# Kernel optimization log

Measured on AMD Instinct MI355X. Metric: run time of the kernel, lower is better.

Reference implementation:

```python
import jax, jax.numpy as jnp
import numpy as np

B, N, E, K = 8, 4096, 1, 3
F = [16, 32, 16]
MLP_HID, MLP_OUT = 64, 1


def graph_filter(x, S, h, b):
    # x: [B, Fin, N], S: [E, N, N], h: [Fout, E, K, Fin], b: [Fout, 1]
    Bx, Fin, Nx = x.shape
    Ex, Kx = h.shape[1], h.shape[2]
    cur = jnp.broadcast_to(x[:, None], (Bx, Ex, Fin, Nx))  # tap 0: z = x
    zs = [cur]
    for _ in range(Kx - 1):
        cur = jnp.einsum('enm,befm->befn', S, cur)  # diffuse one hop
        zs.append(cur)
    z = jnp.stack(zs, axis=2)  # [B, E, K, Fin, N]
    return jnp.einsum('gekf,bekfn->bgn', h, z) + b[None]  # [B, Fout, N]


def gnn_layer(x, S, h, b, n_out):
    # GraphFilter -> ReLU -> NoPool (select first n_out nodes)
    return jax.nn.relu(graph_filter(x, S, h, b))[:, :, :n_out]


def setup_inputs() -> dict:
    key = jax.random.key(0)
    ks = jax.random.split(key, 16)
    sN = np.float32(1.0 / np.sqrt(N))
    x = jax.random.normal(ks[0], (B, F[0], N), dtype=jnp.float32)
    S_clique = jax.random.normal(ks[1], (E, N, N), dtype=jnp.float32) * sN
    S_line = jax.random.normal(ks[2], (E, N, N), dtype=jnp.float32) * sN

    def w(k, fo, fi):
        s = np.float32(1.0 / np.sqrt(fi * K))
        return jax.random.normal(k, (fo, E, K, fi), dtype=jnp.float32) * s

    Wc1, bc1 = w(ks[3], F[1], F[0]), jnp.zeros((F[1], 1), jnp.float32)
    Wc2, bc2 = w(ks[4], F[2], F[1]), jnp.zeros((F[2], 1), jnp.float32)
    Wl1, bl1 = w(ks[5], F[1], F[0]), jnp.zeros((F[1], 1), jnp.float32)
    Wl2, bl2 = w(ks[6], F[2], F[1]), jnp.zeros((F[2], 1), jnp.float32)
    d_in = N * F[-1]
    Wm1 = jax.random.normal(ks[7], (MLP_HID, d_in), dtype=jnp.float32) * np.float32(1.0 / np.sqrt(d_in))
    bm1 = jnp.zeros((MLP_HID,), jnp.float32)
    Wm2 = jax.random.normal(ks[8], (MLP_OUT, MLP_HID), dtype=jnp.float32) * np.float32(1.0 / np.sqrt(MLP_HID))
    bm2 = jnp.zeros((MLP_OUT,), jnp.float32)
    return {'x': x, 'S_clique': S_clique, 'S_line': S_line,
            'Wc1': Wc1, 'bc1': bc1, 'Wc2': Wc2, 'bc2': bc2,
            'Wl1': Wl1, 'bl1': bl1, 'Wl2': Wl2, 'bl2': bl2,
            'Wm1': Wm1, 'bm1': bm1, 'Wm2': Wm2, 'bm2': bm2}


def reference(x, S_clique, S_line, Wc1, bc1, Wc2, bc2, Wl1, bl1, Wl2, bl2, Wm1, bm1, Wm2, bm2):
    # clique-expansion branch (L=2 layers)
    y = gnn_layer(x, S_clique, Wc1, bc1, N)
    y = gnn_layer(y, S_clique, Wc2, bc2, N)
    # line-expansion branch (L=2 layers)
    y = gnn_layer(y, S_line, Wl1, bl1, N)
    y = gnn_layer(y, S_line, Wl2, bl2, N)
    yFlat = y.reshape(y.shape[0], -1)  # [B, F[-1]*N] (row-major matches torch)
    h = jax.nn.relu(yFlat @ Wm1.T + bm1)
    return h @ Wm2.T + bm2  # [B, 1]
```

## Files before the change

### kernel.cpp

```cpp
#include <hip/hip_runtime.h>


#define NN 4096
#define BB 8

typedef unsigned short u16;
typedef unsigned int   u32;

typedef __attribute__((ext_vector_type(8))) short bf16x8;
typedef __attribute__((ext_vector_type(4))) float f32x4;

__device__ __forceinline__ u16 f2bf(float f) {
    union { float f; u32 i; } c; c.f = f;
    u32 i = c.i;
    u32 r = (i + 0x7FFFu + ((i >> 16) & 1u)) >> 16;
    return (u16)r;
}
__device__ __forceinline__ float bf2f(u16 u) {
    union { u32 i; float f; } c; c.i = ((u32)u) << 16; return c.f;
}

__device__ __forceinline__ void gload_lds16(const u16* g, u16* l) {
    __builtin_amdgcn_global_load_lds(
        (__attribute__((address_space(1))) void*)g,
        (__attribute__((address_space(3))) void*)l, 16, 0, 0);
}

__global__ __launch_bounds__(256) void cvt3(const float* __restrict__ a, u16* __restrict__ da, int na,
                                            const float* __restrict__ b, u16* __restrict__ db, int nb,
                                            const float* __restrict__ c, u16* __restrict__ dc, int nc)
{
    const int tot = (na + nb + nc) >> 2;
    for (int q = blockIdx.x * 256 + threadIdx.x; q < tot; q += gridDim.x * 256) {
        const int i = q << 2;
        const float* s; u16* d;
        if (i < na)           { s = a + i;            d = da + i; }
        else if (i < na + nb) { s = b + (i - na);     d = db + (i - na); }
        else                  { s = c + (i - na - nb); d = dc + (i - na - nb); }
        float4 v = *(const float4*)s;
        ushort4 o;
        o.x = f2bf(v.x); o.y = f2bf(v.y); o.z = f2bf(v.z); o.w = f2bf(v.w);
        *(ushort4*)d = o;
    }
}

template <int ITERS>
__global__ __launch_bounds__(256) void diffuse(const u16* __restrict__ Z,
                                               const u16* __restrict__ S,
                                               u16* __restrict__ Part)
{
    __shared__ u16 As[3 * 128 * 64];
    __shared__ u16 Bs[3 * 64 * 64];

    const int bx    = blockIdx.x;
    const int ntile = ((bx & 7) << 3) | (bx >> 3);
    const int nBase = ntile * 64;
    const int mBase = blockIdx.y * 128;
    const int tid   = threadIdx.x;
    const int lane  = tid & 63;
    const int wv    = tid >> 6;
    const int quad  = lane >> 4;
    const int l16   = lane & 15;

    const int kStart = (int)blockIdx.z * (ITERS * 64);

    const int rl   = lane >> 3;
    const int gsl  = lane & 7;
    const int gsrc = gsl ^ rl;

    f32x4 acc[2][4];
#pragma unroll
    for (int i = 0; i < 2; ++i)
#pragma unroll
        for (int j = 0; j < 4; ++j) acc[i][j] = (f32x4){0.f, 0.f, 0.f, 0.f};

    auto stage = [&](int buf, int k0) {
#pragma unroll
        for (int j = 0; j < 4; ++j) {
            const int rb = (wv * 4 + j) * 8;
            gload_lds16(Z + (size_t)(mBase + rb + rl) * NN + k0 + gsrc * 8,
                        &As[buf * 8192 + rb * 64]);
        }
#pragma unroll
        for (int j = 0; j < 2; ++j) {
            const int rb = (wv * 2 + j) * 8;
            gload_lds16(S + (size_t)(nBase + rb + rl) * NN + k0 + gsrc * 8,
                        &Bs[buf * 4096 + rb * 64]);
        }
    };

    auto compute = [&](int buf) {
#pragma unroll
        for (int s = 0; s < 2; ++s) {
            const int g = s * 4 + quad;
            bf16x8 af[2], bf[4];
#pragma unroll
            for (int mi = 0; mi < 2; ++mi) {
                const int r = wv * 32 + mi * 16 + l16;
                af[mi] = *(const bf16x8*)&As[buf * 8192 + r * 64 + ((g ^ (r & 7)) << 3)];
            }
#pragma unroll
            for (int ni = 0; ni < 4; ++ni) {
                const int r = ni * 16 + l16;
                bf[ni] = *(const bf16x8*)&Bs[buf * 4096 + r * 64 + ((g ^ (r & 7)) << 3)];
            }
#pragma unroll
            for (int mi = 0; mi < 2; ++mi)
#pragma unroll
                for (int ni = 0; ni < 4; ++ni)
                    acc[mi][ni] = __builtin_amdgcn_mfma_f32_16x16x32_bf16(
                        af[mi], bf[ni], acc[mi][ni], 0, 0, 0);
        }
    };

    stage(0, kStart);
    stage(1, kStart + 64);

#pragma unroll
    for (int i = 0; i < ITERS; ++i) {
        if (i + 2 < ITERS) stage((i + 2) % 3, kStart + (i + 2) * 64);
        if (i < ITERS - 2)
            asm volatile("s_waitcnt vmcnt(12)" ::: "memory");
        else if (i == ITERS - 2)
            asm volatile("s_waitcnt vmcnt(6)" ::: "memory");
        else
            asm volatile("s_waitcnt vmcnt(0)" ::: "memory");
        __builtin_amdgcn_s_barrier();
        compute(i % 3);
        if (i + 1 < ITERS) __builtin_amdgcn_s_barrier();
    }

    asm volatile("s_waitcnt lgkmcnt(0)" ::: "memory");
    __builtin_amdgcn_s_barrier();

    u16* tb = &As[wv * 2304];
#pragma unroll
    for (int mi = 0; mi < 2; ++mi)
#pragma unroll
        for (int ni = 0; ni < 4; ++ni)
#pragma unroll
            for (int i = 0; i < 4; ++i)
                tb[(mi * 16 + quad * 4 + i) * 72 + ni * 16 + l16] =
                    f2bf(acc[mi][ni][i]);

    const size_t plane = (size_t)gridDim.y * 128 * NN;
    u16* pp = Part + (size_t)blockIdx.z * plane;
    const int row0g = mBase + wv * 32;
#pragma unroll
    for (int j = 0; j < 4; ++j) {
        const int r = (lane >> 3) + j * 8;
        const int c = (lane & 7) * 8;
        bf16x8 v = *(const bf16x8*)&tb[r * 72 + c];
        *(bf16x8*)&pp[(size_t)(row0g + r) * NN + nBase + c] = v;
    }
}

template <int KS>
__global__ __launch_bounds__(256) void reduce_part(const u16* __restrict__ part,
                                                   int planeElems,
                                                   u16* __restrict__ outb)
{
    const int base   = (blockIdx.x * 256 + threadIdx.x) * 8;
    const int stride = gridDim.x * 256 * 8;
    for (int i = base; i < planeElems; i += stride) {
        float s[8];
#pragma unroll
        for (int e = 0; e < 8; ++e) s[e] = 0.f;
#pragma unroll
        for (int p = 0; p < KS; ++p) {
            uint4 v = *(const uint4*)(part + (size_t)p * planeElems + i);
            const u32 w[4] = {v.x, v.y, v.z, v.w};
#pragma unroll
            for (int q = 0; q < 4; ++q) {
                union { u32 i; float f; } lo, hi;
                lo.i = w[q] << 16;
                hi.i = w[q] & 0xFFFF0000u;
                s[q * 2]     += lo.f;
                s[q * 2 + 1] += hi.f;
            }
        }
        uint4 o;
        o.x = (u32)f2bf(s[0]) | ((u32)f2bf(s[1]) << 16);
        o.y = (u32)f2bf(s[2]) | ((u32)f2bf(s[3]) << 16);
        o.z = (u32)f2bf(s[4]) | ((u32)f2bf(s[5]) << 16);
        o.w = (u32)f2bf(s[6]) | ((u32)f2bf(s[7]) << 16);
        *(uint4*)(outb + i) = o;
    }
}

template <int FIN, int FOUT, int KS>
__global__ __launch_bounds__(256) void combine_relu(
    const u16* __restrict__ z0, const u16* __restrict__ z1,
    const u16* __restrict__ part2, int planeElems,
    const float* __restrict__ W, const float* __restrict__ bias,
    u16* __restrict__ out)
{
    __shared__ float hs[FOUT * 3 * FIN];
    __shared__ float bs[FOUT];
    for (int i = threadIdx.x; i < FOUT * 3 * FIN; i += 256) hs[i] = W[i];
    if (threadIdx.x < FOUT) bs[threadIdx.x] = bias[threadIdx.x];
    __syncthreads();

    const int nb = NN / 256;
    const int b  = blockIdx.x / nb;
    const int n  = (blockIdx.x % nb) * 256 + threadIdx.x;

    float zv[3][FIN];
    const u16* zp0 = z0 + (size_t)b * FIN * NN + n;
    const u16* zp1 = z1 + (size_t)b * FIN * NN + n;
    const u16* zp2 = part2 + (size_t)b * FIN * NN + n;
#pragma unroll
    for (int f = 0; f < FIN; ++f) {
        zv[0][f] = bf2f(zp0[(size_t)f * NN]);
        zv[1][f] = bf2f(zp1[(size_t)f * NN]);
        float s = 0.f;
#pragma unroll
        for (int p = 0; p < KS; ++p)
            s += bf2f(zp2[(size_t)p * planeElems + (size_t)f * NN]);
        zv[2][f] = s;
    }

    u16* op = out + (size_t)b * FOUT * NN + n;
    for (int g = 0; g < FOUT; ++g) {
        float acc = bs[g];
#pragma unroll
        for (int k = 0; k < 3; ++k)
#pragma unroll
            for (int f = 0; f < FIN; ++f)
                acc = fmaf(hs[(g * 3 + k) * FIN + f], zv[k][f], acc);
        op[(size_t)g * NN] = f2bf(fmaxf(acc, 0.f));
    }
}

__global__ __launch_bounds__(256) void mlp1(const u16* __restrict__ y,
                                            const float* __restrict__ Wm1,
                                            float* __restrict__ h1p)
{
    const int j    = blockIdx.x;
    const int base = blockIdx.y * 8192;
    const int D    = 16 * NN;

    float acc[BB];
#pragma unroll
    for (int b = 0; b < BB; ++b) acc[b] = 0.f;

    const float* wrow = Wm1 + (size_t)j * D + base;
    for (int idx = threadIdx.x * 8; idx < 8192; idx += 256 * 8) {
        float4 w0 = *(const float4*)(wrow + idx);
        float4 w1 = *(const float4*)(wrow + idx + 4);
#pragma unroll
        for (int b = 0; b < BB; ++b) {
            uint4 yv = *(const uint4*)(y + (size_t)b * D + base + idx);
            union { u32 i; float f; } c[8];
            c[0].i = yv.x << 16; c[1].i = yv.x & 0xFFFF0000u;
            c[2].i = yv.y << 16; c[3].i = yv.y & 0xFFFF0000u;
            c[4].i = yv.z << 16; c[5].i = yv.z & 0xFFFF0000u;
            c[6].i = yv.w << 16; c[7].i = yv.w & 0xFFFF0000u;
            acc[b] = fmaf(w0.x, c[0].f, acc[b]);
            acc[b] = fmaf(w0.y, c[1].f, acc[b]);
            acc[b] = fmaf(w0.z, c[2].f, acc[b]);
            acc[b] = fmaf(w0.w, c[3].f, acc[b]);
            acc[b] = fmaf(w1.x, c[4].f, acc[b]);
            acc[b] = fmaf(w1.y, c[5].f, acc[b]);
            acc[b] = fmaf(w1.z, c[6].f, acc[b]);
            acc[b] = fmaf(w1.w, c[7].f, acc[b]);
        }
    }

    __shared__ float red[BB][4];
    const int lane = threadIdx.x & 63;
    const int w    = threadIdx.x >> 6;
#pragma unroll
    for (int b = 0; b < BB; ++b) {
        float v = acc[b];
        for (int off = 32; off > 0; off >>= 1) v += __shfl_down(v, off, 64);
        if (lane == 0) red[b][w] = v;
    }
    __syncthreads();
    if (threadIdx.x < BB) {
        const int b = threadIdx.x;
        h1p[blockIdx.y * (BB * 64) + b * 64 + j] =
            red[b][0] + red[b][1] + red[b][2] + red[b][3];
    }
}

__global__ void mlp2(const float* __restrict__ h1p,
                     const float* __restrict__ bm1,
                     const float* __restrict__ Wm2,
                     const float* __restrict__ bm2, float* __restrict__ out)
{
    const int lane = threadIdx.x;
    const float w    = Wm2[lane];
    const float b1   = bm1[lane];
    const float bias = bm2[0];
    for (int b = 0; b < BB; ++b) {
        float h = 0.f;
#pragma unroll
        for (int p = 0; p < 8; ++p) h += h1p[p * (BB * 64) + b * 64 + lane];
        float v = fmaxf(h + b1, 0.f) * w;
        for (int off = 32; off > 0; off >>= 1) v += __shfl_down(v, off, 64);
        if (lane == 0) out[b] = v + bias;
    }
}

extern "C" void kernel_launch(void* const* d_in, const int* in_sizes, int n_in,
                              void* d_out, int out_size, void* d_ws, size_t ws_size,
                              hipStream_t stream)
{
    const float* x   = (const float*)d_in[0];
    const float* Sc  = (const float*)d_in[1];
    const float* Sl  = (const float*)d_in[2];
    const float* Wc1 = (const float*)d_in[3];
    const float* bc1 = (const float*)d_in[4];
    const float* Wc2 = (const float*)d_in[5];
    const float* bc2 = (const float*)d_in[6];
    const float* Wl1 = (const float*)d_in[7];
    const float* bl1 = (const float*)d_in[8];
    const float* Wl2 = (const float*)d_in[9];
    const float* bl2 = (const float*)d_in[10];
    const float* Wm1 = (const float*)d_in[11];
    const float* bm1 = (const float*)d_in[12];
    const float* Wm2 = (const float*)d_in[13];
    const float* bm2 = (const float*)d_in[14];
    float* out = (float*)d_out;

    char* ws = (char*)d_ws;
    u16*   part = (u16*)(ws);
    u16*   zb1  = (u16*)(ws + (8u  << 20));
    u16*   yPa  = (u16*)(ws + (12u << 20));
    u16*   yPb  = (u16*)(ws + (14u << 20));
    float* h1p  = (float*)(ws + (16u << 20));
    u16*   Scb  = (u16*)(ws + (17u << 20));
    u16*   Slb  = Scb + (size_t)NN * NN;

    const dim3 blk(256);
    const dim3 gridCmb(BB * NN / 256);
    const dim3 g2(64, 1, 8);
    const dim3 g4(64, 2, 4);
    const int  pl128 = 128 * NN;
    const int  pl256 = 256 * NN;

    cvt3<<<2048, blk, 0, stream>>>(Sc, Scb, NN * NN, Sl, Slb, NN * NN,
                                   x, yPa, 128 * NN);

    diffuse<8><<<g2, blk, 0, stream>>>(yPa, Scb, part);
    reduce_part<8><<<256, blk, 0, stream>>>(part, pl128, zb1);
    diffuse<8><<<g2, blk, 0, stream>>>(zb1, Scb, part);
    combine_relu<16, 32, 8><<<gridCmb, blk, 0, stream>>>(yPa, zb1, part, pl128,
                                                         Wc1, bc1, yPb);
    diffuse<16><<<g4, blk, 0, stream>>>(yPb, Scb, part);
    reduce_part<4><<<512, blk, 0, stream>>>(part, pl256, zb1);
    diffuse<16><<<g4, blk, 0, stream>>>(zb1, Scb, part);
    combine_relu<32, 16, 4><<<gridCmb, blk, 0, stream>>>(yPb, zb1, part, pl256,
                                                         Wc2, bc2, yPa);
    diffuse<8><<<g2, blk, 0, stream>>>(yPa, Slb, part);
    reduce_part<8><<<256, blk, 0, stream>>>(part, pl128, zb1);
    diffuse<8><<<g2, blk, 0, stream>>>(zb1, Slb, part);
    combine_relu<16, 32, 8><<<gridCmb, blk, 0, stream>>>(yPa, zb1, part, pl128,
                                                         Wl1, bl1, yPb);
    diffuse<16><<<g4, blk, 0, stream>>>(yPb, Slb, part);
    reduce_part<4><<<512, blk, 0, stream>>>(part, pl256, zb1);
    diffuse<16><<<g4, blk, 0, stream>>>(zb1, Slb, part);
    combine_relu<32, 16, 4><<<gridCmb, blk, 0, stream>>>(yPb, zb1, part, pl256,
                                                         Wl2, bl2, yPa);
    mlp1<<<dim3(64, 8), blk, 0, stream>>>(yPa, Wm1, h1p);
    mlp2<<<1, 64, 0, stream>>>(h1p, bm1, Wm2, bm2, out);
}
```

Measured before the change: 373.6 us.

## Fuse fp32-to-bf16 conversion of S into first diffusion GEMM per branch

Removes the standalone conversion pass over both shift matrices. Instead, the first diffusion of each branch reads fp32 S directly, converts each tile to bf16 in registers, writes it to LDS for the MFMA, and writes it back to global for later diffusions to reuse. This drops one full read of each fp32 matrix and one separate launch. In exchange the first diffusion uses a register-staged B path with double buffering instead of triple-buffered async LDS loads, and the line-branch conversion now sits after the clique branch instead of up front.

Result: no change. 368.4 us (-1.4%).

```diff
diff --git a/kernel.cpp b/kernel.cpp
--- a/kernel.cpp
+++ b/kernel.cpp
@@ -19,6 +19,9 @@
 __device__ __forceinline__ float bf2f(u16 u) {
     union { u32 i; float f; } c; c.i = ((u32)u) << 16; return c.f;
 }
+__device__ __forceinline__ u32 pack2bf(float lo, float hi) {
+    return (u32)f2bf(lo) | ((u32)f2bf(hi) << 16);
+}
 
 __device__ __forceinline__ void gload_lds16(const u16* g, u16* l) {
     __builtin_amdgcn_global_load_lds(
@@ -26,21 +29,142 @@
         (__attribute__((address_space(3))) void*)l, 16, 0, 0);
 }
 
-__global__ __launch_bounds__(256) void cvt3(const float* __restrict__ a, u16* __restrict__ da, int na,
-                                            const float* __restrict__ b, u16* __restrict__ db, int nb,
-                                            const float* __restrict__ c, u16* __restrict__ dc, int nc)
-{
-    const int tot = (na + nb + nc) >> 2;
-    for (int q = blockIdx.x * 256 + threadIdx.x; q < tot; q += gridDim.x * 256) {
-        const int i = q << 2;
-        const float* s; u16* d;
-        if (i < na)           { s = a + i;            d = da + i; }
-        else if (i < na + nb) { s = b + (i - na);     d = db + (i - na); }
-        else                  { s = c + (i - na - nb); d = dc + (i - na - nb); }
-        float4 v = *(const float4*)s;
-        ushort4 o;
-        o.x = f2bf(v.x); o.y = f2bf(v.y); o.z = f2bf(v.z); o.w = f2bf(v.w);
-        *(ushort4*)d = o;
+__global__ __launch_bounds__(256) void cvt_x(const float* __restrict__ in,
+                                             u16* __restrict__ out)
+{
+    const int i = (blockIdx.x * 256 + threadIdx.x) * 8;
+    float4 a = *(const float4*)(in + i);
+    float4 b = *(const float4*)(in + i + 4);
+    uint4 o;
+    o.x = pack2bf(a.x, a.y); o.y = pack2bf(a.z, a.w);
+    o.z = pack2bf(b.x, b.y); o.w = pack2bf(b.z, b.w);
+    *(uint4*)(out + i) = o;
+}
+
+template <int ITERS>
+__global__ __launch_bounds__(256) void diffuse_cvtB(const u16* __restrict__ Z,
+                                                    const float* __restrict__ Sf,
+                                                    u16* __restrict__ Part,
+                                                    u16* __restrict__ Sb)
+{
+    __shared__ u16 As[2 * 128 * 64];
+    __shared__ u16 Bs[2 * 64 * 64];
+
+    const int bx    = blockIdx.x;
+    const int ntile = ((bx & 7) << 3) | (bx >> 3);
+    const int nBase = ntile * 64;
+    const int mBase = blockIdx.y * 128;
+    const int tid   = threadIdx.x;
+    const int lane  = tid & 63;
+    const int wv    = tid >> 6;
+    const int quad  = lane >> 4;
+    const int l16   = lane & 15;
+
+    const int kStart = (int)blockIdx.z * (ITERS * 64);
+
+    const int rl   = lane >> 3;
+    const int gsl  = lane & 7;
+    const int gsrc = gsl ^ rl;
+
+    f32x4 acc[2][4];
+#pragma unroll
+    for (int i = 0; i < 2; ++i)
+#pragma unroll
+        for (int j = 0; j < 4; ++j) acc[i][j] = (f32x4){0.f, 0.f, 0.f, 0.f};
+
+    auto stageA = [&](int buf, int k0) {
+#pragma unroll
+        for (int j = 0; j < 4; ++j) {
+            const int rb = (wv * 4 + j) * 8;
+            gload_lds16(Z + (size_t)(mBase + rb + rl) * NN + k0 + gsrc * 8,
+                        &As[buf * 8192 + rb * 64]);
+        }
+    };
+
+    float4 fB[2][2];
+    auto loadB = [&](int k0) {
+#pragma unroll
+        for (int j = 0; j < 2; ++j) {
+            const int row = nBase + (wv * 2 + j) * 8 + rl;
+            const float* p = Sf + (size_t)row * NN + k0 + gsrc * 8;
+            fB[j][0] = *(const float4*)p;
+            fB[j][1] = *(const float4*)(p + 4);
+        }
+    };
+    auto writeB = [&](int buf, int k0) {
+#pragma unroll
+        for (int j = 0; j < 2; ++j) {
+            const int rloc = (wv * 2 + j) * 8 + rl;
+            bf16x8 v;
+            v[0] = (short)f2bf(fB[j][0].x); v[1] = (short)f2bf(fB[j][0].y);
+            v[2] = (short)f2bf(fB[j][0].z); v[3] = (short)f2bf(fB[j][0].w);
+            v[4] = (short)f2bf(fB[j][1].x); v[5] = (short)f2bf(fB[j][1].y);
+            v[6] = (short)f2bf(fB[j][1].z); v[7] = (short)f2bf(fB[j][1].w);
+            *(bf16x8*)&Bs[buf * 4096 + rloc * 64 + gsl * 8] = v;
+            *(bf16x8*)&Sb[(size_t)(nBase + rloc) * NN + k0 + gsrc * 8] = v;
+        }
+    };
+
+    auto compute = [&](int buf) {
+#pragma unroll
+        for (int s = 0; s < 2; ++s) {
+            const int g = s * 4 + quad;
+            bf16x8 af[2], bf[4];
+#pragma unroll
+            for (int mi = 0; mi < 2; ++mi) {
+                const int r = wv * 32 + mi * 16 + l16;
+                af[mi] = *(const bf16x8*)&As[buf * 8192 + r * 64 + ((g ^ (r & 7)) << 3)];
+            }
+#pragma unroll
+            for (int ni = 0; ni < 4; ++ni) {
+                const int r = ni * 16 + l16;
+                bf[ni] = *(const bf16x8*)&Bs[buf * 4096 + r * 64 + ((g ^ (r & 7)) << 3)];
+            }
+#pragma unroll
+            for (int mi = 0; mi < 2; ++mi)
+#pragma unroll
+                for (int ni = 0; ni < 4; ++ni)
+                    acc[mi][ni] = __builtin_amdgcn_mfma_f32_16x16x32_bf16(
+                        af[mi], bf[ni], acc[mi][ni], 0, 0, 0);
+        }
+    };
+
+    loadB(kStart);
+    stageA(0, kStart);
+    writeB(0, kStart);
+    __syncthreads();
+
+#pragma unroll
+    for (int i = 0; i < ITERS; ++i) {
+        const int cur = i & 1;
+        if (i + 1 < ITERS) {
+            stageA(cur ^ 1, kStart + (i + 1) * 64);
+            loadB(kStart + (i + 1) * 64);
+        }
+        compute(cur);
+        if (i + 1 < ITERS) writeB(cur ^ 1, kStart + (i + 1) * 64);
+        __syncthreads();
+    }
+
+    u16* tb = &As[wv * 2304];
+#pragma unroll
+    for (int mi = 0; mi < 2; ++mi)
+#pragma unroll
+        for (int ni = 0; ni < 4; ++ni)
+#pragma unroll
+            for (int i = 0; i < 4; ++i)
+                tb[(mi * 16 + quad * 4 + i) * 72 + ni * 16 + l16] =
+                    f2bf(acc[mi][ni][i]);
+
+    const size_t plane = (size_t)gridDim.y * 128 * NN;
+    u16* pp = Part + (size_t)blockIdx.z * plane;
+    const int row0g = mBase + wv * 32;
+#pragma unroll
+    for (int j = 0; j < 4; ++j) {
+        const int r = (lane >> 3) + j * 8;
+        const int c = (lane & 7) * 8;
+        bf16x8 v = *(const bf16x8*)&tb[r * 72 + c];
+        *(bf16x8*)&pp[(size_t)(row0g + r) * NN + nBase + c] = v;
     }
 }
 
@@ -340,10 +464,9 @@
     const int  pl128 = 128 * NN;
     const int  pl256 = 256 * NN;
 
-    cvt3<<<2048, blk, 0, stream>>>(Sc, Scb, NN * NN, Sl, Slb, NN * NN,
-                                   x, yPa, 128 * NN);
-
-    diffuse<8><<<g2, blk, 0, stream>>>(yPa, Scb, part);
+    cvt_x<<<256, blk, 0, stream>>>(x, yPa);
+
+    diffuse_cvtB<8><<<g2, blk, 0, stream>>>(yPa, Sc, part, Scb);
     reduce_part<8><<<256, blk, 0, stream>>>(part, pl128, zb1);
     diffuse<8><<<g2, blk, 0, stream>>>(zb1, Scb, part);
     combine_relu<16, 32, 8><<<gridCmb, blk, 0, stream>>>(yPa, zb1, part, pl128,
@@ -353,7 +476,7 @@
     diffuse<16><<<g4, blk, 0, stream>>>(zb1, Scb, part);
     combine_relu<32, 16, 4><<<gridCmb, blk, 0, stream>>>(yPb, zb1, part, pl256,
                                                          Wc2, bc2, yPa);
-    diffuse<8><<<g2, blk, 0, stream>>>(yPa, Slb, part);
+    diffuse_cvtB<8><<<g2, blk, 0, stream>>>(yPa, Sl, part, Slb);
     reduce_part<8><<<256, blk, 0, stream>>>(part, pl128, zb1);
     diffuse<8><<<g2, blk, 0, stream>>>(zb1, Slb, part);
     combine_relu<16, 32, 8><<<gridCmb, blk, 0, stream>>>(yPa, zb1, part, pl128,
```
